# Performance work log

Measured on AMD Instinct MI355X. Metric: run time of the kernel, lower is better.

## Reference

```python
import jax, jax.numpy as jnp
import numpy as np

B, T, E = 2, 2048, 1024
NEXP, TOPK, INTER = 8, 2, 1408


def setup_inputs() -> dict:
    key = jax.random.key(0)
    ks = jax.random.split(key, 5)
    s = 0.02
    return {
        "x": jax.random.normal(ks[0], (B, T, E), dtype=jnp.float32),
        "gate_w": jax.random.normal(ks[1], (NEXP, E), dtype=jnp.float32) * s,
        "wg": jax.random.normal(ks[2], (NEXP, INTER, E), dtype=jnp.float32) * s,
        "wu": jax.random.normal(ks[3], (NEXP, INTER, E), dtype=jnp.float32) * s,
        "wd": jax.random.normal(ks[4], (NEXP, E, INTER), dtype=jnp.float32) * s,
    }


def reference(x, gate_w, wg, wu, wd):
    # Router: scores [B,T,NEXP], topk softmax over selected experts only
    scores = jnp.einsum("btd,ed->bte", x, gate_w)
    topk_scores, topk_idx = jax.lax.top_k(scores, TOPK)  # [B,T,K]
    topk_probs = jax.nn.softmax(topk_scores, axis=-1)
    # Scatter back to dense gating probs [B,T,NEXP] (topk indices are unique)
    onehot = jax.nn.one_hot(topk_idx, NEXP, dtype=x.dtype)  # [B,T,K,NEXP]
    gating = jnp.sum(onehot * topk_probs[..., None], axis=-2)  # [B,T,NEXP]
    # Dense compute-all-experts (faithful to the original module)
    g = jnp.einsum("btd,eid->btei", x, wg)  # [B,T,NEXP,INTER]
    u = jnp.einsum("btd,eid->btei", x, wu)
    h = jax.nn.silu(g) * u
    expert_out = jnp.einsum("btei,edi->bted", h, wd)  # [B,T,NEXP,E]
    y = jnp.sum(gating[..., None] * expert_out, axis=-2)  # [B,T,E]
    return y
```

## Files before the change

### kernel.cpp

```cpp
#include <hip/hip_runtime.h>
#include <hip/hip_bf16.h>
#include <stdint.h>

typedef __hip_bfloat16 bf16;
typedef __attribute__((ext_vector_type(8))) short short8;
typedef __attribute__((ext_vector_type(4))) float f32x4;

#define NTOK  4096
#define EDIM  1024
#define NEXPT 8
#define INTERD 1408
#define MAXP  4096
#define WELEM (NEXPT * INTERD * EDIM)

#define GL16(g, l) __builtin_amdgcn_global_load_lds( \
    (const __attribute__((address_space(1))) unsigned int*)(g), \
    (__attribute__((address_space(3))) unsigned int*)(l), 16, 0, 0)

#define WAIT_VM(n)   asm volatile("s_waitcnt vmcnt(" #n ")" ::: "memory")
#define BAR()        __builtin_amdgcn_s_barrier()
#define PRIO(n)      __builtin_amdgcn_s_setprio(n)

__global__ __launch_bounds__(256) void cvt3_kernel(const float* __restrict__ wg, bf16* __restrict__ wgb,
                                                   const float* __restrict__ wu, bf16* __restrict__ wub,
                                                   const float* __restrict__ wd, bf16* __restrict__ wdb) {
    const float* src; bf16* dst; int b = blockIdx.x;
    if (b < 1024)      { src = wg; dst = wgb; }
    else if (b < 2048) { src = wu; dst = wub; b -= 1024; }
    else               { src = wd; dst = wdb; b -= 2048; }
    int n = WELEM;
    int i = (b * 256 + threadIdx.x) * 4;
    int stride = 1024 * 256 * 4;
    for (; i < n; i += stride) {
        float4 v = *(const float4*)(src + i);
        ushort4 o; bf16 t;
        t = __float2bfloat16(v.x); o.x = *(unsigned short*)&t;
        t = __float2bfloat16(v.y); o.y = *(unsigned short*)&t;
        t = __float2bfloat16(v.z); o.z = *(unsigned short*)&t;
        t = __float2bfloat16(v.w); o.w = *(unsigned short*)&t;
        *(ushort4*)(dst + i) = o;
    }
}

__global__ __launch_bounds__(256) void router_kernel(const float* __restrict__ x,
                                                     const float* __restrict__ gw,
                                                     bf16* __restrict__ xb,
                                                     int* __restrict__ sel,
                                                     float* __restrict__ tprob) {
    int t = blockIdx.x * 4 + (threadIdx.x >> 6);
    int lane = threadIdx.x & 63;
    const float* xr = x + (size_t)t * EDIM;

    float xv[16];
#pragma unroll
    for (int j = 0; j < 4; j++) {
        float4 v = *(const float4*)(xr + lane * 16 + j * 4);
        xv[4 * j] = v.x; xv[4 * j + 1] = v.y; xv[4 * j + 2] = v.z; xv[4 * j + 3] = v.w;
    }
    bf16* xbr = xb + (size_t)t * EDIM;
#pragma unroll
    for (int j = 0; j < 4; j++) {
        ushort4 o; bf16 c;
        c = __float2bfloat16(xv[4 * j]);     o.x = *(unsigned short*)&c;
        c = __float2bfloat16(xv[4 * j + 1]); o.y = *(unsigned short*)&c;
        c = __float2bfloat16(xv[4 * j + 2]); o.z = *(unsigned short*)&c;
        c = __float2bfloat16(xv[4 * j + 3]); o.w = *(unsigned short*)&c;
        *(ushort4*)(xbr + lane * 16 + j * 4) = o;
    }

    double acc[NEXPT];
#pragma unroll
    for (int e = 0; e < NEXPT; e++) acc[e] = 0.0;
#pragma unroll
    for (int e = 0; e < NEXPT; e++) {
        const float* gr = gw + e * EDIM + lane * 16;
#pragma unroll
        for (int j = 0; j < 16; j++) acc[e] += (double)xv[j] * (double)gr[j];
    }
#pragma unroll
    for (int off = 32; off >= 1; off >>= 1) {
#pragma unroll
        for (int e = 0; e < NEXPT; e++) acc[e] += __shfl_xor(acc[e], off, 64);
    }
    if (lane == 0) {
        int e0 = 0; double s0 = acc[0];
        for (int e = 1; e < NEXPT; e++) if (acc[e] > s0) { s0 = acc[e]; e0 = e; }
        int e1 = -1; double s1 = -1e300;
        for (int e = 0; e < NEXPT; e++) if (e != e0 && acc[e] > s1) { s1 = acc[e]; e1 = e; }
        float z = __expf((float)(s1 - s0));
        float p0 = 1.f / (1.f + z);
        sel[t] = e0 | (e1 << 8);
        tprob[2 * t] = p0;
        tprob[2 * t + 1] = 1.f - p0;
    }
}

__global__ __launch_bounds__(512) void bucket_kernel(const int* __restrict__ sel,
                                                     const float* __restrict__ tprob,
                                                     int* __restrict__ counts,
                                                     int* __restrict__ offsets,
                                                     int* __restrict__ ptok,
                                                     float* __restrict__ pprob,
                                                     int* __restrict__ inv,
                                                     int* __restrict__ wq) {
    __shared__ int scnt[NEXPT];
    int w = threadIdx.x >> 6;
    int lane = threadIdx.x & 63;
    unsigned long long ltmask = (lane == 63) ? ~0ull >> 1 : (1ull << lane) - 1;
    int base = 0;
    for (int t0 = 0; t0 < NTOK; t0 += 64) {
        int t = t0 + lane;
        int s = sel[t];
        int e0 = s & 0xff, e1 = (s >> 8) & 0xff;
        unsigned long long m0 = __ballot(e0 == w);
        if (e0 == w) {
            int pos = base + __popcll(m0 & ltmask);
            ptok[w * MAXP + pos] = t;
            pprob[w * MAXP + pos] = tprob[2 * t];
            inv[2 * t] = (w << 16) | pos;
        }
        base += __popcll(m0);
        unsigned long long m1 = __ballot(e1 == w);
        if (e1 == w) {
            int pos = base + __popcll(m1 & ltmask);
            ptok[w * MAXP + pos] = t;
            pprob[w * MAXP + pos] = tprob[2 * t + 1];
            inv[2 * t + 1] = (w << 16) | pos;
        }
        base += __popcll(m1);
    }
    if (lane == 0) scnt[w] = base;
    __syncthreads();
    if (threadIdx.x < NEXPT) {
        int off = 0;
        for (int e = 0; e < (int)threadIdx.x; e++) off += scnt[e];
        counts[threadIdx.x] = scnt[threadIdx.x];
        offsets[threadIdx.x] = off;
        wq[threadIdx.x] = 0;
    }
}

__global__ __launch_bounds__(512, 4) void gemm1_kernel(const bf16* __restrict__ xb,
                                                       const bf16* __restrict__ wgb,
                                                       const bf16* __restrict__ wub,
                                                       bf16* __restrict__ hout,
                                                       const int* __restrict__ counts,
                                                       const int* __restrict__ offsets,
                                                       const int* __restrict__ ptok,
                                                       const float* __restrict__ pprob,
                                                       int* __restrict__ wq) {
    int e = blockIdx.x & 7;
    int cnt = counts[e];
    int hbase = offsets[e];
    int mtiles = (cnt + 127) >> 7;
    int tiles = mtiles * (INTERD / 128);

    __shared__ __align__(16) bf16 smem[3 * 12288];
    __shared__ int s_wi;

    int tid  = threadIdx.x;
    int lane = tid & 63;
    int wid  = tid >> 6;
    int wm   = wid >> 2;
    int wn   = wid & 3;

    int srow = tid >> 2;
    int qs   = (((tid & 3) ^ ((srow >> 1) & 3)) * 8);
    int l15  = lane & 15;
    int l4   = lane >> 4;

    int offA[4], offG[2];
#pragma unroll
    for (int m = 0; m < 4; m++) {
        int r = wm * 64 + m * 16 + l15;
        offA[m] = r * 32 + ((l4 ^ ((r >> 1) & 3)) * 8);
    }
#pragma unroll
    for (int n = 0; n < 2; n++) {
        int r = wn * 32 + n * 16 + l15;
        offG[n] = r * 32 + ((l4 ^ ((r >> 1) & 3)) * 8);
    }

    for (;;) {
        if (tid == 0) s_wi = atomicAdd(&wq[e], 1);
        __syncthreads();
        int wi = s_wi;
        if (wi >= tiles) break;
        int mt = wi % mtiles;
        int nt = wi / mtiles;
        int m0 = mt * 128;
        int n0 = nt * 128;

        WAIT_VM(0);
        const bf16* gA = xb + (size_t)ptok[e * MAXP + min(m0 + srow, cnt - 1)] * EDIM + qs;
        const bf16* gG = wgb + ((size_t)e * INTERD + n0 + srow) * EDIM + qs;
        const bf16* gU = wub + ((size_t)e * INTERD + n0 + srow) * EDIM + qs;

        f32x4 accg[4][2], accu[4][2];
#pragma unroll
        for (int m = 0; m < 4; m++)
#pragma unroll
            for (int n = 0; n < 2; n++) {
                accg[m][n] = (f32x4){0.f, 0.f, 0.f, 0.f};
                accu[m][n] = (f32x4){0.f, 0.f, 0.f, 0.f};
            }

#define SB1(t) (smem + ((t) % 3) * 12288)
#define G1_STAGE(t) do { bf16* sb_ = SB1(t); int ko_ = (t) * 32; \
        GL16(gA + ko_, sb_ + wid * 512); \
        GL16(gG + ko_, sb_ + 4096 + wid * 512); \
        GL16(gU + ko_, sb_ + 8192 + wid * 512); } while (0)

        G1_STAGE(0); G1_STAGE(1);

        for (int t = 0; t < 32; ++t) {
            if (t < 30)       { G1_STAGE(t + 2); WAIT_VM(6); }
            else if (t == 30) { WAIT_VM(3); }
            else              { WAIT_VM(0); }
            BAR();
            const bf16* sb = SB1(t);
            short8 a_[4], gf[2], uf[2];
#pragma unroll
            for (int m = 0; m < 4; m++) a_[m] = *(const short8*)&sb[offA[m]];
#pragma unroll
            for (int n = 0; n < 2; n++) {
                gf[n] = *(const short8*)&sb[4096 + offG[n]];
                uf[n] = *(const short8*)&sb[8192 + offG[n]];
            }
            PRIO(1);
#pragma unroll
            for (int m = 0; m < 4; m++)
#pragma unroll
                for (int n = 0; n < 2; n++) {
                    accg[m][n] = __builtin_amdgcn_mfma_f32_16x16x32_bf16(a_[m], gf[n], accg[m][n], 0, 0, 0);
                    accu[m][n] = __builtin_amdgcn_mfma_f32_16x16x32_bf16(a_[m], uf[n], accu[m][n], 0, 0, 0);
                }
            PRIO(0);
            BAR();
        }
#undef SB1
#undef G1_STAGE

#pragma unroll
        for (int m = 0; m < 4; m++)
#pragma unroll
            for (int n = 0; n < 2; n++)
#pragma unroll
                for (int r = 0; r < 4; r++) {
                    int pos = m0 + wm * 64 + m * 16 + l4 * 4 + r;
                    if (pos < cnt) {
                        int col = n0 + wn * 32 + n * 16 + l15;
                        float p = pprob[e * MAXP + pos];
                        float gv = accg[m][n][r];
                        float uv = accu[m][n][r];
                        float hv = (gv / (1.f + __expf(-gv))) * uv * p;
                        hout[(size_t)(hbase + pos) * INTERD + col] = __float2bfloat16(hv);
                    }
                }
    }
}

__global__ __launch_bounds__(512, 4) void gemm2_kernel(const bf16* __restrict__ h,
                                                       const bf16* __restrict__ wdb,
                                                       float* __restrict__ out2,
                                                       const int* __restrict__ counts,
                                                       const int* __restrict__ offsets) {
    int bx = blockIdx.x;
    int e  = bx & 7;
    int mt = (bx >> 3) & 7;
    int nt = bx >> 6;
    int cnt = counts[e];
    int n0 = nt * 256;
    int hbase = offsets[e];

    __shared__ __align__(16) bf16 smem[3 * 12288];

    int tid  = threadIdx.x;
    int lane = tid & 63;
    int wid  = tid >> 6;
    int wm   = wid >> 2;
    int wn   = wid & 3;

    int srow = tid >> 2;
    int qs   = (((tid & 3) ^ ((srow >> 1) & 3)) * 8);
    int l15  = lane & 15;
    int l4   = lane >> 4;

    int offA[4], offB[4];
#pragma unroll
    for (int m = 0; m < 4; m++) {
        int r = wm * 64 + m * 16 + l15;
        offA[m] = r * 32 + ((l4 ^ ((r >> 1) & 3)) * 8);
    }
#pragma unroll
    for (int n = 0; n < 4; n++) {
        int r = wn * 64 + n * 16 + l15;
        offB[n] = 4096 + r * 32 + ((l4 ^ ((r >> 1) & 3)) * 8);
    }

    const bf16* gB0 = wdb + ((size_t)e * EDIM + n0 + srow) * INTERD + qs;
    const bf16* gB1 = wdb + ((size_t)e * EDIM + n0 + 128 + srow) * INTERD + qs;

    for (int m0 = mt * 128; m0 < cnt; m0 += 1024) {
        WAIT_VM(0);
        const bf16* gA = h + (size_t)(hbase + min(m0 + srow, cnt - 1)) * INTERD + qs;

        f32x4 acc[4][4];
#pragma unroll
        for (int m = 0; m < 4; m++)
#pragma unroll
            for (int n = 0; n < 4; n++) acc[m][n] = (f32x4){0.f, 0.f, 0.f, 0.f};

#define SB2(t) (smem + ((t) % 3) * 12288)
#define G2_STAGE(t) do { bf16* sb_ = SB2(t); int ko_ = (t) * 32; \
        GL16(gA + ko_,  sb_ + wid * 512); \
        GL16(gB0 + ko_, sb_ + 4096 + wid * 512); \
        GL16(gB1 + ko_, sb_ + 8192 + wid * 512); } while (0)

        G2_STAGE(0); G2_STAGE(1);

        for (int t = 0; t < 44; ++t) {
            if (t < 42)       { G2_STAGE(t + 2); WAIT_VM(6); }
            else if (t == 42) { WAIT_VM(3); }
            else              { WAIT_VM(0); }
            BAR();
            const bf16* sb = SB2(t);
            short8 a_[4], b_[4];
#pragma unroll
            for (int m = 0; m < 4; m++) a_[m] = *(const short8*)&sb[offA[m]];
#pragma unroll
            for (int n = 0; n < 4; n++) b_[n] = *(const short8*)&sb[offB[n]];
            PRIO(1);
#pragma unroll
            for (int m = 0; m < 4; m++)
#pragma unroll
                for (int n = 0; n < 4; n++)
                    acc[m][n] = __builtin_amdgcn_mfma_f32_16x16x32_bf16(a_[m], b_[n], acc[m][n], 0, 0, 0);
            PRIO(0);
            BAR();
        }
#undef SB2
#undef G2_STAGE

#pragma unroll
        for (int m = 0; m < 4; m++)
#pragma unroll
            for (int n = 0; n < 4; n++)
#pragma unroll
                for (int r = 0; r < 4; r++) {
                    int pos = m0 + wm * 64 + m * 16 + l4 * 4 + r;
                    if (pos < cnt) {
                        int col = n0 + wn * 64 + n * 16 + l15;
                        out2[(size_t)(hbase + pos) * EDIM + col] = acc[m][n][r];
                    }
                }
    }
}

__global__ __launch_bounds__(256) void combine_kernel(const float* __restrict__ out2,
                                                      const int* __restrict__ inv,
                                                      const int* __restrict__ offsets,
                                                      float* __restrict__ y) {
    int idx = blockIdx.x * 256 + threadIdx.x;
    int t = idx >> 8;
    int c = (idx & 255) * 4;
    int a = inv[2 * t], b = inv[2 * t + 1];
    size_t sa = (size_t)(offsets[a >> 16] + (a & 0xFFFF)) * EDIM + c;
    size_t sb = (size_t)(offsets[b >> 16] + (b & 0xFFFF)) * EDIM + c;
    float4 va = *(const float4*)(out2 + sa);
    float4 vb = *(const float4*)(out2 + sb);
    float4 o;
    o.x = va.x + vb.x; o.y = va.y + vb.y; o.z = va.z + vb.z; o.w = va.w + vb.w;
    *(float4*)(y + (size_t)t * EDIM + c) = o;
}

extern "C" void kernel_launch(void* const* d_in, const int* in_sizes, int n_in,
                              void* d_out, int out_size, void* d_ws, size_t ws_size,
                              hipStream_t stream) {
    const float* x      = (const float*)d_in[0];
    const float* gate_w = (const float*)d_in[1];
    const float* wg     = (const float*)d_in[2];
    const float* wu     = (const float*)d_in[3];
    const float* wd     = (const float*)d_in[4];
    float* y = (float*)d_out;

    char* ws = (char*)d_ws;
    constexpr size_t SZ_XB = (size_t)NTOK * EDIM * 2;
    constexpr size_t SZ_W  = (size_t)WELEM * 2;
    constexpr size_t SZ_H  = (size_t)NTOK * 2 * INTERD * 2;
    bf16* xb  = (bf16*)ws;
    bf16* wgb = (bf16*)(ws + SZ_XB);
    bf16* wub = (bf16*)(ws + SZ_XB + SZ_W);
    bf16* wdb = (bf16*)(ws + SZ_XB + 2 * SZ_W);
    bf16* h   = (bf16*)(ws + SZ_XB + 3 * SZ_W);
    char* meta = ws + SZ_XB + 3 * SZ_W + SZ_H;
    int*   counts  = (int*)meta;
    int*   offsets = (int*)(meta + 256);
    int*   ptok    = (int*)(meta + 512);
    float* pprob   = (float*)(meta + 512 + (size_t)NEXPT * MAXP * 4);
    int*   inv     = (int*)(meta + 512 + (size_t)NEXPT * MAXP * 8);
    int*   wq      = (int*)(meta + 512 + (size_t)NEXPT * MAXP * 8 + (size_t)NTOK * 2 * 4);
    int*   sel     = (int*)(meta + 512 + (size_t)NEXPT * MAXP * 8 + (size_t)NTOK * 2 * 4 + 256);
    float* tprob   = (float*)((char*)sel + (size_t)NTOK * 4);
    float* out2 = (float*)(ws + SZ_XB);

    cvt3_kernel<<<3072, 256, 0, stream>>>(wg, wgb, wu, wub, wd, wdb);
    router_kernel<<<NTOK / 4, 256, 0, stream>>>(x, gate_w, xb, sel, tprob);
    bucket_kernel<<<1, 512, 0, stream>>>(sel, tprob, counts, offsets, ptok, pprob, inv, wq);

    gemm1_kernel<<<512, 512, 0, stream>>>(
        xb, wgb, wub, h, counts, offsets, ptok, pprob, wq);
    gemm2_kernel<<<NEXPT * 8 * (EDIM / 256), 512, 0, stream>>>(
        h, wdb, out2, counts, offsets);
    combine_kernel<<<NTOK * EDIM / 4 / 256, 256, 0, stream>>>(out2, inv, offsets, y);
}
```

Before: 224.5 us.

## Fuse prep kernels, add work-stealing across experts, shrink tiles, store bf16 expert outputs

Merges weight conversion and routing into one launch. Both GEMMs now use a per-expert atomic work queue in which blocks steal tiles from other experts. The queue counters are padded onto separate cache lines. Pipelining drops from three LDS stages to two and gemm2 tiles shrink to 128x128, so occupancy bounds can rise, and gemm1 launches more blocks. Expert outputs are stored as bf16 to halve the out2 write and the combine read, at the cost of extra rounding before the final sum.

```diff
diff --git a/kernel.cpp b/kernel.cpp
--- a/kernel.cpp
+++ b/kernel.cpp
@@ -21,36 +21,36 @@
 #define BAR()        __builtin_amdgcn_s_barrier()
 #define PRIO(n)      __builtin_amdgcn_s_setprio(n)
 
-__global__ __launch_bounds__(256) void cvt3_kernel(const float* __restrict__ wg, bf16* __restrict__ wgb,
+__global__ __launch_bounds__(256) void prep_kernel(const float* __restrict__ wg, bf16* __restrict__ wgb,
                                                    const float* __restrict__ wu, bf16* __restrict__ wub,
-                                                   const float* __restrict__ wd, bf16* __restrict__ wdb) {
-    const float* src; bf16* dst; int b = blockIdx.x;
-    if (b < 1024)      { src = wg; dst = wgb; }
-    else if (b < 2048) { src = wu; dst = wub; b -= 1024; }
-    else               { src = wd; dst = wdb; b -= 2048; }
-    int n = WELEM;
-    int i = (b * 256 + threadIdx.x) * 4;
-    int stride = 1024 * 256 * 4;
-    for (; i < n; i += stride) {
-        float4 v = *(const float4*)(src + i);
-        ushort4 o; bf16 t;
-        t = __float2bfloat16(v.x); o.x = *(unsigned short*)&t;
-        t = __float2bfloat16(v.y); o.y = *(unsigned short*)&t;
-        t = __float2bfloat16(v.z); o.z = *(unsigned short*)&t;
-        t = __float2bfloat16(v.w); o.w = *(unsigned short*)&t;
-        *(ushort4*)(dst + i) = o;
-    }
-}
-
-__global__ __launch_bounds__(256) void router_kernel(const float* __restrict__ x,
-                                                     const float* __restrict__ gw,
-                                                     bf16* __restrict__ xb,
-                                                     int* __restrict__ sel,
-                                                     float* __restrict__ tprob) {
-    int t = blockIdx.x * 4 + (threadIdx.x >> 6);
+                                                   const float* __restrict__ wd, bf16* __restrict__ wdb,
+                                                   const float* __restrict__ x,
+                                                   const float* __restrict__ gw,
+                                                   bf16* __restrict__ xb,
+                                                   int* __restrict__ sel,
+                                                   float* __restrict__ tprob) {
+    int b = blockIdx.x;
+    if (b < 3072) {
+        const float* src; bf16* dst;
+        if (b < 1024)      { src = wg; dst = wgb; }
+        else if (b < 2048) { src = wu; dst = wub; b -= 1024; }
+        else               { src = wd; dst = wdb; b -= 2048; }
+        int i = (b * 256 + threadIdx.x) * 4;
+        int stride = 1024 * 256 * 4;
+        for (; i < WELEM; i += stride) {
+            float4 v = *(const float4*)(src + i);
+            ushort4 o; bf16 t;
+            t = __float2bfloat16(v.x); o.x = *(unsigned short*)&t;
+            t = __float2bfloat16(v.y); o.y = *(unsigned short*)&t;
+            t = __float2bfloat16(v.z); o.z = *(unsigned short*)&t;
+            t = __float2bfloat16(v.w); o.w = *(unsigned short*)&t;
+            *(ushort4*)(dst + i) = o;
+        }
+        return;
+    }
+    int t = (b - 3072) * 4 + (threadIdx.x >> 6);
     int lane = threadIdx.x & 63;
     const float* xr = x + (size_t)t * EDIM;
-
     float xv[16];
 #pragma unroll
     for (int j = 0; j < 4; j++) {
@@ -67,7 +67,6 @@
         c = __float2bfloat16(xv[4 * j + 3]); o.w = *(unsigned short*)&c;
         *(ushort4*)(xbr + lane * 16 + j * 4) = o;
     }
-
     double acc[NEXPT];
 #pragma unroll
     for (int e = 0; e < NEXPT; e++) acc[e] = 0.0;
@@ -102,7 +101,8 @@
                                                      int* __restrict__ ptok,
                                                      float* __restrict__ pprob,
                                                      int* __restrict__ inv,
-                                                     int* __restrict__ wq) {
+                                                     int* __restrict__ wq1,
+                                                     int* __restrict__ wq2) {
     __shared__ int scnt[NEXPT];
     int w = threadIdx.x >> 6;
     int lane = threadIdx.x & 63;
@@ -136,11 +136,12 @@
         for (int e = 0; e < (int)threadIdx.x; e++) off += scnt[e];
         counts[threadIdx.x] = scnt[threadIdx.x];
         offsets[threadIdx.x] = off;
-        wq[threadIdx.x] = 0;
-    }
-}
-
-__global__ __launch_bounds__(512, 4) void gemm1_kernel(const bf16* __restrict__ xb,
+        wq1[threadIdx.x * 32] = 0;
+        wq2[threadIdx.x * 32] = 0;
+    }
+}
+
+__global__ __launch_bounds__(512, 6) void gemm1_kernel(const bf16* __restrict__ xb,
                                                        const bf16* __restrict__ wgb,
                                                        const bf16* __restrict__ wub,
                                                        bf16* __restrict__ hout,
@@ -148,14 +149,10 @@
                                                        const int* __restrict__ offsets,
                                                        const int* __restrict__ ptok,
                                                        const float* __restrict__ pprob,
-                                                       int* __restrict__ wq) {
-    int e = blockIdx.x & 7;
-    int cnt = counts[e];
-    int hbase = offsets[e];
-    int mtiles = (cnt + 127) >> 7;
-    int tiles = mtiles * (INTERD / 128);
-
-    __shared__ __align__(16) bf16 smem[3 * 12288];
+                                                       int* __restrict__ wq1) {
+    int eown = blockIdx.x & 7;
+
+    __shared__ __align__(16) bf16 smem[2 * 12288];
     __shared__ int s_wi;
 
     int tid  = threadIdx.x;
@@ -181,99 +178,103 @@
         offG[n] = r * 32 + ((l4 ^ ((r >> 1) & 3)) * 8);
     }
 
-    for (;;) {
-        if (tid == 0) s_wi = atomicAdd(&wq[e], 1);
-        __syncthreads();
-        int wi = s_wi;
-        if (wi >= tiles) break;
-        int mt = wi % mtiles;
-        int nt = wi / mtiles;
-        int m0 = mt * 128;
-        int n0 = nt * 128;
-
-        WAIT_VM(0);
-        const bf16* gA = xb + (size_t)ptok[e * MAXP + min(m0 + srow, cnt - 1)] * EDIM + qs;
-        const bf16* gG = wgb + ((size_t)e * INTERD + n0 + srow) * EDIM + qs;
-        const bf16* gU = wub + ((size_t)e * INTERD + n0 + srow) * EDIM + qs;
-
-        f32x4 accg[4][2], accu[4][2];
-#pragma unroll
-        for (int m = 0; m < 4; m++)
-#pragma unroll
-            for (int n = 0; n < 2; n++) {
-                accg[m][n] = (f32x4){0.f, 0.f, 0.f, 0.f};
-                accu[m][n] = (f32x4){0.f, 0.f, 0.f, 0.f};
+    for (int ei = 0; ei < NEXPT; ++ei) {
+        int e = (eown + ei) & 7;
+        int cnt = counts[e];
+        int mtiles = (cnt + 127) >> 7;
+        int tiles = mtiles * (INTERD / 128);
+        int hbase = offsets[e];
+
+        for (;;) {
+            if (tid == 0) s_wi = atomicAdd(&wq1[e * 32], 1);
+            __syncthreads();
+            int wi = s_wi;
+            __syncthreads();
+            if (wi >= tiles) break;
+            int mt = wi % mtiles;
+            int nt = wi / mtiles;
+            int m0 = mt * 128;
+            int n0 = nt * 128;
+
+            WAIT_VM(0);
+            const bf16* gA = xb + (size_t)ptok[e * MAXP + min(m0 + srow, cnt - 1)] * EDIM + qs;
+            const bf16* gG = wgb + ((size_t)e * INTERD + n0 + srow) * EDIM + qs;
+            const bf16* gU = wub + ((size_t)e * INTERD + n0 + srow) * EDIM + qs;
+
+            f32x4 accg[4][2], accu[4][2];
+#pragma unroll
+            for (int m = 0; m < 4; m++)
+#pragma unroll
+                for (int n = 0; n < 2; n++) {
+                    accg[m][n] = (f32x4){0.f, 0.f, 0.f, 0.f};
+                    accu[m][n] = (f32x4){0.f, 0.f, 0.f, 0.f};
+                }
+
+#define SB1(t) (smem + ((t) & 1) * 12288)
+#define G1_STAGE(t) do { bf16* sb_ = SB1(t); int ko_ = (t) * 32; \
+            GL16(gA + ko_, sb_ + wid * 512); \
+            GL16(gG + ko_, sb_ + 4096 + wid * 512); \
+            GL16(gU + ko_, sb_ + 8192 + wid * 512); } while (0)
+
+            G1_STAGE(0);
+
+            for (int t = 0; t < 32; ++t) {
+                if (t < 31) { G1_STAGE(t + 1); WAIT_VM(3); }
+                else        { WAIT_VM(0); }
+                BAR();
+                const bf16* sb = SB1(t);
+                short8 a_[4], gf[2], uf[2];
+#pragma unroll
+                for (int m = 0; m < 4; m++) a_[m] = *(const short8*)&sb[offA[m]];
+#pragma unroll
+                for (int n = 0; n < 2; n++) {
+                    gf[n] = *(const short8*)&sb[4096 + offG[n]];
+                    uf[n] = *(const short8*)&sb[8192 + offG[n]];
+                }
+                PRIO(1);
+#pragma unroll
+                for (int m = 0; m < 4; m++)
+#pragma unroll
+                    for (int n = 0; n < 2; n++) {
+                        accg[m][n] = __builtin_amdgcn_mfma_f32_16x16x32_bf16(a_[m], gf[n], accg[m][n], 0, 0, 0);
+                        accu[m][n] = __builtin_amdgcn_mfma_f32_16x16x32_bf16(a_[m], uf[n], accu[m][n], 0, 0, 0);
+                    }
+                PRIO(0);
+                BAR();
             }
-
-#define SB1(t) (smem + ((t) % 3) * 12288)
-#define G1_STAGE(t) do { bf16* sb_ = SB1(t); int ko_ = (t) * 32; \
-        GL16(gA + ko_, sb_ + wid * 512); \
-        GL16(gG + ko_, sb_ + 4096 + wid * 512); \
-        GL16(gU + ko_, sb_ + 8192 + wid * 512); } while (0)
-
-        G1_STAGE(0); G1_STAGE(1);
-
-        for (int t = 0; t < 32; ++t) {
-            if (t < 30)       { G1_STAGE(t + 2); WAIT_VM(6); }
-            else if (t == 30) { WAIT_VM(3); }
-            else              { WAIT_VM(0); }
-            BAR();
-            const bf16* sb = SB1(t);
-            short8 a_[4], gf[2], uf[2];
-#pragma unroll
-            for (int m = 0; m < 4; m++) a_[m] = *(const short8*)&sb[offA[m]];
-#pragma unroll
-            for (int n = 0; n < 2; n++) {
-                gf[n] = *(const short8*)&sb[4096 + offG[n]];
-                uf[n] = *(const short8*)&sb[8192 + offG[n]];
-            }
-            PRIO(1);
-#pragma unroll
-            for (int m = 0; m < 4; m++)
-#pragma unroll
-                for (int n = 0; n < 2; n++) {
-                    accg[m][n] = __builtin_amdgcn_mfma_f32_16x16x32_bf16(a_[m], gf[n], accg[m][n], 0, 0, 0);
-                    accu[m][n] = __builtin_amdgcn_mfma_f32_16x16x32_bf16(a_[m], uf[n], accu[m][n], 0, 0, 0);
-                }
-            PRIO(0);
-            BAR();
-        }
 #undef SB1
 #undef G1_STAGE
 
 #pragma unroll
-        for (int m = 0; m < 4; m++)
-#pragma unroll
-            for (int n = 0; n < 2; n++)
-#pragma unroll
-                for (int r = 0; r < 4; r++) {
-                    int pos = m0 + wm * 64 + m * 16 + l4 * 4 + r;
-                    if (pos < cnt) {
-                        int col = n0 + wn * 32 + n * 16 + l15;
-                        float p = pprob[e * MAXP + pos];
-                        float gv = accg[m][n][r];
-                        float uv = accu[m][n][r];
-                        float hv = (gv / (1.f + __expf(-gv))) * uv * p;
-                        hout[(size_t)(hbase + pos) * INTERD + col] = __float2bfloat16(hv);
+            for (int m = 0; m < 4; m++)
+#pragma unroll
+                for (int n = 0; n < 2; n++)
+#pragma unroll
+                    for (int r = 0; r < 4; r++) {
+                        int pos = m0 + wm * 64 + m * 16 + l4 * 4 + r;
+                        if (pos < cnt) {
+                            int col = n0 + wn * 32 + n * 16 + l15;
+                            float p = pprob[e * MAXP + pos];
+                            float gv = accg[m][n][r];
+                            float uv = accu[m][n][r];
+                            float hv = (gv / (1.f + __expf(-gv))) * uv * p;
+                            hout[(size_t)(hbase + pos) * INTERD + col] = __float2bfloat16(hv);
+                        }
                     }
-                }
-    }
-}
-
-__global__ __launch_bounds__(512, 4) void gemm2_kernel(const bf16* __restrict__ h,
+        }
+    }
+}
+
+__global__ __launch_bounds__(512, 8) void gemm2_kernel(const bf16* __restrict__ h,
                                                        const bf16* __restrict__ wdb,
-                                                       float* __restrict__ out2,
+                                                       bf16* __restrict__ out2,
                                                        const int* __restrict__ counts,
-                                                       const int* __restrict__ offsets) {
-    int bx = blockIdx.x;
-    int e  = bx & 7;
-    int mt = (bx >> 3) & 7;
-    int nt = bx >> 6;
-    int cnt = counts[e];
-    int n0 = nt * 256;
-    int hbase = offsets[e];
-
-    __shared__ __align__(16) bf16 smem[3 * 12288];
+                                                       const int* __restrict__ offsets,
+                                                       int* __restrict__ wq2) {
+    int eown = blockIdx.x & 7;
+
+    __shared__ __align__(16) bf16 smem[2 * 8192];
+    __shared__ int s_wi;
 
     int tid  = threadIdx.x;
     int lane = tid & 63;
@@ -286,92 +287,111 @@
     int l15  = lane & 15;
     int l4   = lane >> 4;
 
-    int offA[4], offB[4];
+    int offA[4], offB[2];
 #pragma unroll
     for (int m = 0; m < 4; m++) {
         int r = wm * 64 + m * 16 + l15;
         offA[m] = r * 32 + ((l4 ^ ((r >> 1) & 3)) * 8);
     }
 #pragma unroll
-    for (int n = 0; n < 4; n++) {
-        int r = wn * 64 + n * 16 + l15;
+    for (int n = 0; n < 2; n++) {
+        int r = wn * 32 + n * 16 + l15;
         offB[n] = 4096 + r * 32 + ((l4 ^ ((r >> 1) & 3)) * 8);
     }
 
-    const bf16* gB0 = wdb + ((size_t)e * EDIM + n0 + srow) * INTERD + qs;
-    const bf16* gB1 = wdb + ((size_t)e * EDIM + n0 + 128 + srow) * INTERD + qs;
-
-    for (int m0 = mt * 128; m0 < cnt; m0 += 1024) {
-        WAIT_VM(0);
-        const bf16* gA = h + (size_t)(hbase + min(m0 + srow, cnt - 1)) * INTERD + qs;
-
-        f32x4 acc[4][4];
-#pragma unroll
-        for (int m = 0; m < 4; m++)
-#pragma unroll
-            for (int n = 0; n < 4; n++) acc[m][n] = (f32x4){0.f, 0.f, 0.f, 0.f};
-
-#define SB2(t) (smem + ((t) % 3) * 12288)
+    for (int ei = 0; ei < NEXPT; ++ei) {
+        int e = (eown + ei) & 7;
+        int cnt = counts[e];
+        int mtiles = (cnt + 127) >> 7;
+        int tiles = mtiles * (EDIM / 128);
+        int hbase = offsets[e];
+
+        for (;;) {
+            if (tid == 0) s_wi = atomicAdd(&wq2[e * 32], 1);
+            __syncthreads();
+            int wi = s_wi;
+            __syncthreads();
+            if (wi >= tiles) break;
+            int mt = wi % mtiles;
+            int nt = wi / mtiles;
+            int m0 = mt * 128;
+            int n0 = nt * 128;
+
+            WAIT_VM(0);
+            const bf16* gA = h + (size_t)(hbase + min(m0 + srow, cnt - 1)) * INTERD + qs;
+            const bf16* gB = wdb + ((size_t)e * EDIM + n0 + srow) * INTERD + qs;
+
+            f32x4 acc[4][2];
+#pragma unroll
+            for (int m = 0; m < 4; m++)
+#pragma unroll
+                for (int n = 0; n < 2; n++) acc[m][n] = (f32x4){0.f, 0.f, 0.f, 0.f};
+
+#define SB2(t) (smem + ((t) & 1) * 8192)
 #define G2_STAGE(t) do { bf16* sb_ = SB2(t); int ko_ = (t) * 32; \
-        GL16(gA + ko_,  sb_ + wid * 512); \
-        GL16(gB0 + ko_, sb_ + 4096 + wid * 512); \
-        GL16(gB1 + ko_, sb_ + 8192 + wid * 512); } while (0)
-
-        G2_STAGE(0); G2_STAGE(1);
-
-        for (int t = 0; t < 44; ++t) {
-            if (t < 42)       { G2_STAGE(t + 2); WAIT_VM(6); }
-            else if (t == 42) { WAIT_VM(3); }
-            else              { WAIT_VM(0); }
-            BAR();
-            const bf16* sb = SB2(t);
-            short8 a_[4], b_[4];
-#pragma unroll
-            for (int m = 0; m < 4; m++) a_[m] = *(const short8*)&sb[offA[m]];
-#pragma unroll
-            for (int n = 0; n < 4; n++) b_[n] = *(const short8*)&sb[offB[n]];
-            PRIO(1);
-#pragma unroll
-            for (int m = 0; m < 4; m++)
-#pragma unroll
-                for (int n = 0; n < 4; n++)
-                    acc[m][n] = __builtin_amdgcn_mfma_f32_16x16x32_bf16(a_[m], b_[n], acc[m][n], 0, 0, 0);
-            PRIO(0);
-            BAR();
-        }
+            GL16(gA + ko_, sb_ + wid * 512); \
+            GL16(gB + ko_, sb_ + 4096 + wid * 512); } while (0)
+
+            G2_STAGE(0);
+
+            for (int t = 0; t < 44; ++t) {
+                if (t < 43) { G2_STAGE(t + 1); WAIT_VM(2); }
+                else        { WAIT_VM(0); }
+                BAR();
+                const bf16* sb = SB2(t);
+                short8 a_[4], b_[2];
+#pragma unroll
+                for (int m = 0; m < 4; m++) a_[m] = *(const short8*)&sb[offA[m]];
+#pragma unroll
+                for (int n = 0; n < 2; n++) b_[n] = *(const short8*)&sb[offB[n]];
+                PRIO(1);
+#pragma unroll
+                for (int m = 0; m < 4; m++)
+#pragma unroll
+                    for (int n = 0; n < 2; n++)
+                        acc[m][n] = __builtin_amdgcn_mfma_f32_16x16x32_bf16(a_[m], b_[n], acc[m][n], 0, 0, 0);
+                PRIO(0);
+                BAR();
+            }
 #undef SB2
 #undef G2_STAGE
 
 #pragma unroll
-        for (int m = 0; m < 4; m++)
-#pragma unroll
-            for (int n = 0; n < 4; n++)
-#pragma unroll
-                for (int r = 0; r < 4; r++) {
-                    int pos = m0 + wm * 64 + m * 16 + l4 * 4 + r;
-                    if (pos < cnt) {
-                        int col = n0 + wn * 64 + n * 16 + l15;
-                        out2[(size_t)(hbase + pos) * EDIM + col] = acc[m][n][r];
+            for (int m = 0; m < 4; m++)
+#pragma unroll
+                for (int n = 0; n < 2; n++)
+#pragma unroll
+                    for (int r = 0; r < 4; r++) {
+                        int pos = m0 + wm * 64 + m * 16 + l4 * 4 + r;
+                        if (pos < cnt) {
+                            int col = n0 + wn * 32 + n * 16 + l15;
+                            out2[(size_t)(hbase + pos) * EDIM + col] = __float2bfloat16(acc[m][n][r]);
+                        }
                     }
-                }
-    }
-}
-
-__global__ __launch_bounds__(256) void combine_kernel(const float* __restrict__ out2,
+        }
+    }
+}
+
+__global__ __launch_bounds__(256) void combine_kernel(const bf16* __restrict__ out2,
                                                       const int* __restrict__ inv,
                                                       const int* __restrict__ offsets,
                                                       float* __restrict__ y) {
     int idx = blockIdx.x * 256 + threadIdx.x;
-    int t = idx >> 8;
-    int c = (idx & 255) * 4;
+    int t = idx >> 7;
+    int c = (idx & 127) * 8;
     int a = inv[2 * t], b = inv[2 * t + 1];
-    size_t sa = (size_t)(offsets[a >> 16] + (a & 0xFFFF)) * EDIM + c;
-    size_t sb = (size_t)(offsets[b >> 16] + (b & 0xFFFF)) * EDIM + c;
-    float4 va = *(const float4*)(out2 + sa);
-    float4 vb = *(const float4*)(out2 + sb);
-    float4 o;
-    o.x = va.x + vb.x; o.y = va.y + vb.y; o.z = va.z + vb.z; o.w = va.w + vb.w;
-    *(float4*)(y + (size_t)t * EDIM + c) = o;
+    const short8 va = *(const short8*)(out2 + (size_t)(offsets[a >> 16] + (a & 0xFFFF)) * EDIM + c);
+    const short8 vb = *(const short8*)(out2 + (size_t)(offsets[b >> 16] + (b & 0xFFFF)) * EDIM + c);
+    float o[8];
+#pragma unroll
+    for (int j = 0; j < 8; j++) {
+        unsigned ua = ((unsigned)(unsigned short)va[j]) << 16;
+        unsigned ub = ((unsigned)(unsigned short)vb[j]) << 16;
+        o[j] = *(float*)&ua + *(float*)&ub;
+    }
+    float* yp = y + (size_t)t * EDIM + c;
+    *(float4*)yp       = (float4){o[0], o[1], o[2], o[3]};
+    *(float4*)(yp + 4) = (float4){o[4], o[5], o[6], o[7]};
 }
 
 extern "C" void kernel_launch(void* const* d_in, const int* in_sizes, int n_in,
@@ -399,18 +419,21 @@
     int*   ptok    = (int*)(meta + 512);
     float* pprob   = (float*)(meta + 512 + (size_t)NEXPT * MAXP * 4);
     int*   inv     = (int*)(meta + 512 + (size_t)NEXPT * MAXP * 8);
-    int*   wq      = (int*)(meta + 512 + (size_t)NEXPT * MAXP * 8 + (size_t)NTOK * 2 * 4);
-    int*   sel     = (int*)(meta + 512 + (size_t)NEXPT * MAXP * 8 + (size_t)NTOK * 2 * 4 + 256);
-    float* tprob   = (float*)((char*)sel + (size_t)NTOK * 4);
-    float* out2 = (float*)(ws + SZ_XB);
-
-    cvt3_kernel<<<3072, 256, 0, stream>>>(wg, wgb, wu, wub, wd, wdb);
-    router_kernel<<<NTOK / 4, 256, 0, stream>>>(x, gate_w, xb, sel, tprob);
-    bucket_kernel<<<1, 512, 0, stream>>>(sel, tprob, counts, offsets, ptok, pprob, inv, wq);
-
-    gemm1_kernel<<<512, 512, 0, stream>>>(
-        xb, wgb, wub, h, counts, offsets, ptok, pprob, wq);
-    gemm2_kernel<<<NEXPT * 8 * (EDIM / 256), 512, 0, stream>>>(
-        h, wdb, out2, counts, offsets);
-    combine_kernel<<<NTOK * EDIM / 4 / 256, 256, 0, stream>>>(out2, inv, offsets, y);
-}
+    char*  meta2   = meta + 512 + (size_t)NEXPT * MAXP * 8 + (size_t)NTOK * 2 * 4;
+    int*   wq1     = (int*)meta2;
+    int*   wq2     = (int*)(meta2 + 1024);
+    int*   sel     = (int*)(meta2 + 2048);
+    float* tprob   = (float*)(meta2 + 2048 + (size_t)NTOK * 4);
+    bf16* out2 = (bf16*)(ws + SZ_XB);
+
+    prep_kernel<<<3072 + NTOK / 4, 256, 0, stream>>>(wg, wgb, wu, wub, wd, wdb,
+                                                     x, gate_w, xb, sel, tprob);
+    bucket_kernel<<<1, 512, 0, stream>>>(sel, tprob, counts, offsets, ptok, pprob, inv,
+                                         wq1, wq2);
+
+    gemm1_kernel<<<768, 512, 0, stream>>>(
+        xb, wgb, wub, h, counts, offsets, ptok, pprob, wq1);
+    gemm2_kernel<<<1024, 512, 0, stream>>>(
+        h, wdb, out2, counts, offsets, wq2);
+    combine_kernel<<<NTOK * EDIM / 8 / 256, 256, 0, stream>>>(out2, inv, offsets, y);
+}
```

Result: slower. 609.7 us (+171.5%).
